# Kernel tuning notes

Measured on AMD Instinct MI355X. Metric: run time of the kernel, lower is better.

Reference implementation:

```python
import jax, jax.numpy as jnp
import numpy as np

B, S, D = 128, 1024, 256
K = 512  # num_clusters


def setup_inputs() -> dict:
    key = jax.random.key(0)
    k1, = jax.random.split(key, 1)
    inputs = jax.random.normal(k1, (B, S, D), dtype=jnp.float32)
    # init centroids as the first K data points so no cluster is empty
    centroids = inputs.reshape(-1, D)[:K]
    return {"inputs": inputs, "centroids": centroids}


def reference(inputs, centroids):
    d = inputs.shape[-1]
    k = centroids.shape[0]
    x = inputs.reshape(-1, d)                      # [N, D]
    # squared euclidean distances via GEMM decomposition (avoids N x K x D tensor)
    x2 = jnp.sum(x * x, axis=1, keepdims=True)     # [N, 1]
    c2 = jnp.sum(centroids * centroids, axis=1)    # [K]
    dist = x2 - 2.0 * (x @ centroids.T) + c2       # [N, K]
    idx = jnp.argmin(dist, axis=-1)                # [N]
    clusters = jax.nn.one_hot(idx, k, dtype=x.dtype)   # [N, K]
    counts = jnp.sum(clusters, axis=0)             # [K]
    sums = jnp.einsum('nk,nd->kd', clusters, x)    # [K, D] scatter-reduce as GEMM
    new_centroids = sums / counts[:, None]         # [K, D]
    updated_centroids = 0.9 * centroids + 0.1 * new_centroids  # EMA update
    clusters_out = clusters.reshape(inputs.shape[:-1] + (k,))  # [B, S, K]
    return clusters_out, updated_centroids
```

## Files before the change

### kernel.cpp

```cpp
#include <hip/hip_runtime.h>
#include <hip/hip_fp16.h>

#define NPTS 131072
#define DIM  256
#define KTOT 512
#define GAP_PAIR 0.2f
#define GAP_FULL 0.4f

typedef unsigned short u16;
typedef _Float16 half8 __attribute__((ext_vector_type(8)));
typedef float floatx4 __attribute__((ext_vector_type(4)));

union F16U { _Float16 f; unsigned short u; };

#define WS_MAIN_NEED 8394816u

__device__ __forceinline__ void ins2(float v, int k, float& B, int& KB, float& S, int& KS) {
  if (v < B || (v == B && k < KB)) { S = B; KS = KB; B = v; KB = k; }
  else if (v < S || (v == S && k < KS)) { S = v; KS = k; }
}

__global__ __launch_bounds__(64)
void c2_kernel(const float* __restrict__ c, double* __restrict__ c2) {
  int k = blockIdx.x;
  int lane = threadIdx.x;
  const float* row = c + (size_t)k * DIM;
  double s = 0.0;
#pragma unroll
  for (int r = 0; r < DIM / 64; ++r) {
    float v = row[r * 64 + lane];
    s += (double)v * (double)v;
  }
#pragma unroll
  for (int off = 32; off > 0; off >>= 1) s += __shfl_down(s, off);
  if (lane == 0) c2[k] = s;
}

__global__ __launch_bounds__(64)
void prep_c_kernel(const float* __restrict__ c, double* __restrict__ c2,
                   u16* __restrict__ Ch, float* __restrict__ cT) {
  int k = blockIdx.x, lane = threadIdx.x;
  const float* row = c + (size_t)k * DIM;
  float4 v = ((const float4*)row)[lane];
  double s = (double)v.x * v.x + (double)v.y * v.y + (double)v.z * v.z + (double)v.w * v.w;
#pragma unroll
  for (int off = 32; off > 0; off >>= 1) s += __shfl_down(s, off);
  if (lane == 0) c2[k] = s;
  cT[(size_t)(lane * 4 + 0) * KTOT + k] = v.x;
  cT[(size_t)(lane * 4 + 1) * KTOT + k] = v.y;
  cT[(size_t)(lane * 4 + 2) * KTOT + k] = v.z;
  cT[(size_t)(lane * 4 + 3) * KTOT + k] = v.w;
  int cg = lane >> 1, h = lane & 1;
  int kc = cg >> 3, cc = cg & 7;
  union { _Float16 hh[4]; ushort4 u; } cvt;
  cvt.hh[0] = (_Float16)v.x; cvt.hh[1] = (_Float16)v.y;
  cvt.hh[2] = (_Float16)v.z; cvt.hh[3] = (_Float16)v.w;
  *(ushort4*)(Ch + (size_t)k * DIM + kc * 64 + (size_t)(cc ^ (k & 7)) * 8 + h * 4) = cvt.u;
}

__device__ __forceinline__ void load_lds16(const void* g, void* l) {
  __builtin_amdgcn_global_load_lds((const __attribute__((address_space(1))) void*)g,
                                   (__attribute__((address_space(3))) void*)l, 16, 0, 0);
}

__global__ __launch_bounds__(256)
void gemm_topk_kernel(const float* __restrict__ x, const u16* __restrict__ Ch,
                      const double* __restrict__ c2,
                      float* __restrict__ pv1, int* __restrict__ pkk, unsigned* __restrict__ pgg) {
  __shared__ __align__(16) u16 Ah[128 * 64];
  __shared__ __align__(16) u16 Bh[128 * 64];
  __shared__ float mb[128][2], msv[128][2], mbf[128];
  __shared__ int mkb[128][2], mks[128][2], scnt[128][2];

  const int tid = threadIdx.x;
  const int bx = blockIdx.x;
  const int nblk = (bx >> 3) & 3;
  const int mblk = (bx & 7) + ((bx >> 5) << 3);
  const int m0 = mblk * 128, n0 = nblk * 128;
  const int w = tid >> 6, lane = tid & 63;
  const int wm = (w & 1) * 64, wn = (w >> 1) * 64;
  const int lm = lane & 15, quad = lane >> 4;

  floatx4 acc[4][4] = {};

  for (int kc = 0; kc < 4; ++kc) {
    const int k0 = kc * 64;
    __syncthreads();
#pragma unroll
    for (int i = 0; i < 4; ++i) {
      int s = i * 256 + tid;
      int row = s >> 3, pos = s & 7;
      size_t go = (size_t)(n0 + row) * DIM + k0 + pos * 8;
      load_lds16(Ch + go, Bh + (size_t)s * 8);
    }
#pragma unroll
    for (int i = 0; i < 4; ++i) {
      int s = i * 256 + tid;
      int row = s >> 3, kg = s & 7;
      const float4* gx = (const float4*)(x + (size_t)(m0 + row) * DIM + k0 + kg * 8);
      float4 f0 = gx[0], f1 = gx[1];
      float fv[8] = {f0.x, f0.y, f0.z, f0.w, f1.x, f1.y, f1.z, f1.w};
      half8 hv;
#pragma unroll
      for (int e = 0; e < 8; ++e) hv[e] = (_Float16)fv[e];
      int pos = kg ^ (row & 7);
      *(half8*)(Ah + (size_t)row * 64 + pos * 8) = hv;
    }
    __syncthreads();

#pragma unroll
    for (int s = 0; s < 2; ++s) {
      half8 ah[4], bh[4];
#pragma unroll
      for (int t = 0; t < 4; ++t) {
        int m = wm + t * 16 + lm;
        int pa = ((s * 4 + quad) ^ (m & 7)) * 8;
        ah[t] = *(const half8*)(Ah + (size_t)m * 64 + pa);
        int n = wn + t * 16 + lm;
        int pb = ((s * 4 + quad) ^ (n & 7)) * 8;
        bh[t] = *(const half8*)(Bh + (size_t)n * 64 + pb);
      }
#pragma unroll
      for (int mt = 0; mt < 4; ++mt)
#pragma unroll
        for (int nt = 0; nt < 4; ++nt)
          acc[mt][nt] = __builtin_amdgcn_mfma_f32_16x16x32_f16(ah[mt], bh[nt], acc[mt][nt], 0, 0, 0);
    }
  }

  float c2f[4];
#pragma unroll
  for (int nt = 0; nt < 4; ++nt) c2f[nt] = (float)c2[n0 + wn + nt * 16 + lm];

  __syncthreads();
#pragma unroll
  for (int mt = 0; mt < 4; ++mt)
#pragma unroll
    for (int r = 0; r < 4; ++r) {
      float bv = 1e30f, sv = 1e30f;
      int bk = 0x7fffffff, sk = 0x7fffffff;
#pragma unroll
      for (int nt = 0; nt < 4; ++nt) {
        float v = c2f[nt] - 2.0f * acc[mt][nt][r];
        int n = n0 + wn + nt * 16 + lm;
        if (v < bv || (v == bv && n < bk)) { sv = bv; sk = bk; bv = v; bk = n; }
        else if (v < sv || (v == sv && n < sk)) { sv = v; sk = n; }
      }
#pragma unroll
      for (int off = 1; off < 16; off <<= 1) {
        float ov = __shfl_xor(bv, off), osv = __shfl_xor(sv, off);
        int ok = __shfl_xor(bk, off), osk = __shfl_xor(sk, off);
        if (ov < bv || (ov == bv && ok < bk)) {
          if (bv < osv || (bv == osv && bk < osk)) { sv = bv; sk = bk; }
          else { sv = osv; sk = osk; }
          bv = ov; bk = ok;
        } else if (ov < sv || (ov == sv && ok < sk)) { sv = ov; sk = ok; }
      }
      if (lm == 0) {
        int mr = wm + mt * 16 + quad * 4 + r;
        int sl = w >> 1;
        mb[mr][sl] = bv; mkb[mr][sl] = bk; msv[mr][sl] = sv; mks[mr][sl] = sk;
      }
    }
  __syncthreads();
  if (tid < 128) {
    float B = mb[tid][0], S = msv[tid][0];
    int KB = mkb[tid][0], KS = mks[tid][0];
    ins2(mb[tid][1], mkb[tid][1], B, KB, S, KS);
    ins2(msv[tid][1], mks[tid][1], B, KB, S, KS);
    mb[tid][0] = B; mkb[tid][0] = KB; msv[tid][0] = S; mks[tid][0] = KS;
    mbf[tid] = B;
  }
  __syncthreads();
#pragma unroll
  for (int mt = 0; mt < 4; ++mt)
#pragma unroll
    for (int r = 0; r < 4; ++r) {
      int mr = wm + mt * 16 + quad * 4 + r;
      float thr = mbf[mr] + GAP_FULL;
      int cnt = 0;
#pragma unroll
      for (int nt = 0; nt < 4; ++nt)
        cnt += (c2f[nt] - 2.0f * acc[mt][nt][r] < thr) ? 1 : 0;
#pragma unroll
      for (int off = 1; off < 16; off <<= 1) cnt += __shfl_xor(cnt, off);
      if (lm == 0) scnt[mr][w >> 1] = cnt;
    }
  __syncthreads();
  if (tid < 128) {
    float B = mb[tid][0], S = msv[tid][0];
    int KB = mkb[tid][0], KS = mks[tid][0];
    int C = scnt[tid][0] + scnt[tid][1];
    int m = m0 + tid;
    F16U cv; cv.f = (_Float16)(S - B);
    pv1[(size_t)nblk * NPTS + m] = B;
    pkk[(size_t)nblk * NPTS + m] = KB | (KS << 16);
    pgg[(size_t)nblk * NPTS + m] = (unsigned)cv.u | ((unsigned)C << 16);
  }
}

__global__ __launch_bounds__(256)
void combine_kernel(const float* __restrict__ pv1, const int* __restrict__ pkk,
                    const unsigned* __restrict__ pgg, int* __restrict__ idx,
                    int* __restrict__ flagcnt, int* __restrict__ flaglist,
                    int* __restrict__ counts) {
  __shared__ int h[KTOT];
  int t = threadIdx.x;
#pragma unroll
  for (int i = 0; i < KTOT / 256; ++i) h[i * 256 + t] = 0;
  __syncthreads();
  int m = blockIdx.x * 256 + t;
  float B = 1e30f, S = 1e30f;
  int KB = 0x7fffffff, KS = 0x7fffffff;
  float bb[4]; int cc[4];
#pragma unroll
  for (int b = 0; b < 4; ++b) {
    float bv = pv1[(size_t)b * NPTS + m];
    int kk = pkk[(size_t)b * NPTS + m];
    unsigned gg = pgg[(size_t)b * NPTS + m];
    int kb_ = kk & 0xffff, ks_ = (kk >> 16) & 0xffff;
    F16U cv; cv.u = (unsigned short)(gg & 0xffffu);
    float sv = bv + (float)cv.f;
    bb[b] = bv; cc[b] = (int)(gg >> 16);
    ins2(bv, kb_, B, KB, S, KS);
    ins2(sv, ks_, B, KB, S, KS);
  }
  idx[m] = KB;
  atomicAdd(&h[KB], 1);
  int tot = 0;
#pragma unroll
  for (int b = 0; b < 4; ++b)
    if (bb[b] < B + GAP_FULL) tot += cc[b];
  if (tot >= 3) {
    int p = atomicAdd(&flagcnt[0], 1);
    if (p < 32768) flaglist[p] = m;
  } else if (tot == 2 && (S - B) < GAP_PAIR) {
    int p = atomicAdd(&flagcnt[1], 1);
    if (p < 32768) {
      flaglist[32768 + p] = m;
      flaglist[65536 + p] = KB | (KS << 16);
    }
  }
  __syncthreads();
#pragma unroll
  for (int i = 0; i < KTOT / 256; ++i) {
    int v = h[i * 256 + t];
    if (v) atomicAdd(&counts[i * 256 + t], v);
  }
}

__global__ __launch_bounds__(256)
void pair_refine_kernel(const float* __restrict__ x, const float* __restrict__ c,
                        const double* __restrict__ c2, const int* __restrict__ flagcnt,
                        const int* __restrict__ flaglist, int* __restrict__ idx,
                        int* __restrict__ counts) {
  int cnt = *(volatile const int*)(flagcnt + 1);
  const int w = threadIdx.x >> 6, lane = threadIdx.x & 63;
  for (int e = blockIdx.x * 4 + w; e < cnt; e += gridDim.x * 4) {
    int m = flaglist[32768 + e];
    int kk = flaglist[65536 + e];
    int ka = kk & 0xffff, kb = (kk >> 16) & 0xffff;
    float4 xv = ((const float4*)(x + (size_t)m * DIM))[lane];
    float4 av = ((const float4*)(c + (size_t)ka * DIM))[lane];
    float4 bv = ((const float4*)(c + (size_t)kb * DIM))[lane];
    float fa = fmaf(xv.x, av.x, fmaf(xv.y, av.y, fmaf(xv.z, av.z, xv.w * av.w)));
    float fb = fmaf(xv.x, bv.x, fmaf(xv.y, bv.y, fmaf(xv.z, bv.z, xv.w * bv.w)));
    double da = (double)fa, db = (double)fb;
#pragma unroll
    for (int off = 32; off > 0; off >>= 1) {
      da += __shfl_down(da, off);
      db += __shfl_down(db, off);
    }
    if (lane == 0) {
      double sa = c2[ka] - 2.0 * da, sb = c2[kb] - 2.0 * db;
      int wk = (sb < sa || (sb == sa && kb < ka)) ? kb : ka;
      if (wk != ka) {
        idx[m] = wk;
        atomicSub(&counts[ka], 1);
        atomicAdd(&counts[wk], 1);
      }
    }
  }
}

__global__ __launch_bounds__(256)
void full_refine_kernel(const float* __restrict__ x, const float* __restrict__ cT,
                        const double* __restrict__ c2, const int* __restrict__ flagcnt,
                        const int* __restrict__ flaglist, int* __restrict__ idx,
                        int* __restrict__ counts) {
  __shared__ __align__(16) float xs[DIM];
  __shared__ double rv[256];
  __shared__ int rk[256];
  int cnt = *(volatile const int*)flagcnt;
  const int ka = threadIdx.x, kb = threadIdx.x + 256;
  for (int i = blockIdx.x; i < cnt; i += gridDim.x) {
    __syncthreads();
    int m = flaglist[i];
    if (threadIdx.x < 64)
      ((float4*)xs)[threadIdx.x] = ((const float4*)(x + (size_t)m * DIM))[threadIdx.x];
    __syncthreads();
    double da = 0.0, db = 0.0;
#pragma unroll
    for (int dc = 0; dc < 8; ++dc) {
      float fa = 0.0f, fb = 0.0f;
#pragma unroll
      for (int d4 = 0; d4 < 8; ++d4) {
        float4 xv = ((const float4*)xs)[dc * 8 + d4];
        const float* ct0 = cT + (size_t)(dc * 32 + d4 * 4) * KTOT;
        fa = fmaf(xv.x, ct0[ka], fa);            fb = fmaf(xv.x, ct0[kb], fb);
        fa = fmaf(xv.y, ct0[KTOT + ka], fa);     fb = fmaf(xv.y, ct0[KTOT + kb], fb);
        fa = fmaf(xv.z, ct0[2 * KTOT + ka], fa); fb = fmaf(xv.z, ct0[2 * KTOT + kb], fb);
        fa = fmaf(xv.w, ct0[3 * KTOT + ka], fa); fb = fmaf(xv.w, ct0[3 * KTOT + kb], fb);
      }
      da += (double)fa; db += (double)fb;
    }
    double sa = c2[ka] - 2.0 * da, sb = c2[kb] - 2.0 * db;
    double bestv; int bestk;
    if (sa <= sb) { bestv = sa; bestk = ka; }
    else          { bestv = sb; bestk = kb; }
    rv[threadIdx.x] = bestv; rk[threadIdx.x] = bestk;
    __syncthreads();
    for (int off = 128; off > 0; off >>= 1) {
      if (threadIdx.x < off) {
        double v = rv[threadIdx.x + off]; int kk = rk[threadIdx.x + off];
        if (v < rv[threadIdx.x] || (v == rv[threadIdx.x] && kk < rk[threadIdx.x])) {
          rv[threadIdx.x] = v; rk[threadIdx.x] = kk;
        }
      }
      __syncthreads();
    }
    if (threadIdx.x == 0) {
      int bk = rk[0];
      int old = idx[m];
      if (bk != old) {
        idx[m] = bk;
        atomicSub(&counts[old], 1);
        atomicAdd(&counts[bk], 1);
      }
    }
  }
}

__global__ __launch_bounds__(256)
void onehot_kernel(const int* __restrict__ idx, float* __restrict__ out) {
  __shared__ int bk[32];
  int b = blockIdx.x;
  if (threadIdx.x < 32) bk[threadIdx.x] = idx[b * 32 + threadIdx.x];
  __syncthreads();
  float4* o = (float4*)(out + (size_t)b * 32 * KTOT);
#pragma unroll
  for (int j = 0; j < 16; ++j) {
    int f4 = j * 256 + threadIdx.x;
    int p = f4 >> 7;
    int n4 = (f4 & 127) * 4;
    int k = bk[p];
    float4 v;
    v.x = (k == n4 + 0) ? 1.0f : 0.0f;
    v.y = (k == n4 + 1) ? 1.0f : 0.0f;
    v.z = (k == n4 + 2) ? 1.0f : 0.0f;
    v.w = (k == n4 + 3) ? 1.0f : 0.0f;
    o[f4] = v;
  }
}

__global__ __launch_bounds__(512)
void scan_kernel(const int* __restrict__ counts, int* __restrict__ offsets,
                 int* __restrict__ cursors) {
  __shared__ int s[KTOT];
  int t = threadIdx.x;
  int mine = counts[t];
  s[t] = mine;
  __syncthreads();
  for (int off = 1; off < KTOT; off <<= 1) {
    int v = (t >= off) ? s[t - off] : 0;
    __syncthreads();
    s[t] += v;
    __syncthreads();
  }
  int excl = s[t] - mine;
  offsets[t] = excl;
  cursors[t] = excl;
  if (t == KTOT - 1) offsets[KTOT] = s[t];
}

__global__ __launch_bounds__(256)
void scatter_kernel(const int* __restrict__ idx, int* __restrict__ cursors,
                    int* __restrict__ plist) {
  int base = blockIdx.x * 1024 + threadIdx.x;
#pragma unroll
  for (int j = 0; j < 4; ++j) {
    int n = base + j * 256;
    int k = idx[n];
    int pos = atomicAdd(&cursors[k], 1);
    plist[pos] = n;
  }
}

__global__ __launch_bounds__(256)
void gathersum_flat_kernel(const float* __restrict__ x, const int* __restrict__ plist,
                           const int* __restrict__ offsets, float* __restrict__ sums) {
  __shared__ int offs[KTOT + 1];
  for (int t = threadIdx.x; t < KTOT + 1; t += 256) offs[t] = offsets[t];
  __syncthreads();
  const int w = threadIdx.x >> 6, lane = threadIdx.x & 63;
  const int wid = blockIdx.x * 4 + w;
  const int p0 = wid * 32, p1 = p0 + 32;

  int lo = 0, hi = KTOT;
  while (hi - lo > 1) { int mid = (lo + hi) >> 1; if (offs[mid] <= p0) lo = mid; else hi = mid; }
  int k = lo;

  float4 acc = make_float4(0.f, 0.f, 0.f, 0.f);
  bool any = false;
#pragma unroll 4
  for (int i = p0; i < p1; ++i) {
    while (i >= offs[k + 1]) {
      if (any) {
        float* dst = sums + (size_t)k * DIM + lane * 4;
        atomicAdd(dst + 0, acc.x); atomicAdd(dst + 1, acc.y);
        atomicAdd(dst + 2, acc.z); atomicAdd(dst + 3, acc.w);
        acc = make_float4(0.f, 0.f, 0.f, 0.f);
        any = false;
      }
      ++k;
    }
    int pid = plist[i];
    float4 v = ((const float4*)x)[(size_t)pid * 64 + lane];
    acc.x += v.x; acc.y += v.y; acc.z += v.z; acc.w += v.w;
    any = true;
  }
  if (any) {
    float* dst = sums + (size_t)k * DIM + lane * 4;
    atomicAdd(dst + 0, acc.x); atomicAdd(dst + 1, acc.y);
    atomicAdd(dst + 2, acc.z); atomicAdd(dst + 3, acc.w);
  }
}

__global__ __launch_bounds__(256)
void ema_kernel(const float* __restrict__ c, const float* __restrict__ sums,
                const int* __restrict__ counts, float* __restrict__ outc) {
  int k = blockIdx.x;
  int d = threadIdx.x;
  float cnt = (float)counts[k];
  size_t o = (size_t)k * DIM + d;
  float nc = sums[o] / cnt;
  outc[o] = 0.9f * c[o] + 0.1f * nc;
}

#define GB 4
#define SLICES 8
__global__ __launch_bounds__(256)
void sums_kernel(const float* __restrict__ x, const int* __restrict__ idx,
                 float* __restrict__ sums, int* __restrict__ counts) {
  const int groups = KTOT / GB;
  const int group = blockIdx.x % groups;
  const int slice = blockIdx.x / groups;
  const int kg0 = group * GB;
  const int tid = threadIdx.x;
  const int lane = tid & 63;
  const int w = tid >> 6;
  const int per_slice = NPTS / SLICES;
  const int nbeg = slice * per_slice;

  float4 acc[GB];
  int cnt[GB];
#pragma unroll
  for (int j = 0; j < GB; ++j) { acc[j] = make_float4(0.f, 0.f, 0.f, 0.f); cnt[j] = 0; }

  for (int it = 0; it < per_slice; it += 256) {
    int n = nbeg + it + tid;
    int k = idx[n];
#pragma unroll
    for (int j = 0; j < GB; ++j) {
      unsigned long long m = __ballot(k == kg0 + j);
      while (m) {
        int src = __ffsll((unsigned long long)m) - 1;
        int nn = __shfl(n, src);
        float4 v = ((const float4*)(x + (size_t)nn * DIM))[lane];
        acc[j].x += v.x; acc[j].y += v.y; acc[j].z += v.z; acc[j].w += v.w;
        cnt[j]++;
        m &= (m - 1);
      }
    }
  }

  __shared__ __align__(16) float lacc[4][GB][DIM];
  __shared__ int lcnt[4][GB];
#pragma unroll
  for (int j = 0; j < GB; ++j) ((float4*)&lacc[w][j][0])[lane] = acc[j];
  if (lane == 0) {
#pragma unroll
    for (int j = 0; j < GB; ++j) lcnt[w][j] = cnt[j];
  }
  __syncthreads();
#pragma unroll
  for (int j = 0; j < GB; ++j) {
    float s = lacc[0][j][tid] + lacc[1][j][tid] + lacc[2][j][tid] + lacc[3][j][tid];
    atomicAdd(&sums[(size_t)(kg0 + j) * DIM + tid], s);
  }
  if (tid < GB) {
    int ct = lcnt[0][tid] + lcnt[1][tid] + lcnt[2][tid] + lcnt[3][tid];
    atomicAdd(&counts[kg0 + tid], ct);
  }
}

#define MP 64
#define KT 64
#define DT 32
__global__ __launch_bounds__(256, 2)
void assign_kernel_r1(const float* __restrict__ x, const float* __restrict__ c,
                      const double* __restrict__ c2, float* __restrict__ out,
                      int* __restrict__ idx_out) {
  __shared__ __align__(16) float xs[DIM * MP];
  __shared__ __align__(16) float cs[DT * KT];
  const int tid = threadIdx.x;
  const int p0 = blockIdx.x * MP;
  const int tp = tid & 15;
  const int tk = tid >> 4;
  {
    const int p = tid >> 2;
    const int dg = tid & 3;
    const float4* x4 = (const float4*)(x + (size_t)(p0 + p) * DIM);
#pragma unroll
    for (int r = 0; r < 16; ++r) {
      int d4 = r * 4 + dg;
      float4 v = x4[d4];
      int dbase = d4 * 4;
      xs[(dbase + 0) * MP + p] = v.x;
      xs[(dbase + 1) * MP + p] = v.y;
      xs[(dbase + 2) * MP + p] = v.z;
      xs[(dbase + 3) * MP + p] = v.w;
    }
  }
  double best[4]; int bestk[4];
#pragma unroll
  for (int i = 0; i < 4; ++i) { best[i] = 1e300; bestk[i] = 0; }
  for (int kc = 0; kc < KTOT / KT; ++kc) {
    const int k0 = kc * KT;
    double dacc[4][4];
#pragma unroll
    for (int i = 0; i < 4; ++i)
#pragma unroll
      for (int j = 0; j < 4; ++j) dacc[i][j] = 0.0;
    for (int dc = 0; dc < DIM / DT; ++dc) {
      __syncthreads();
      {
        const int kl = tid >> 2;
        const int dg = tid & 3;
        const float4* c4 = (const float4*)(c + (size_t)(k0 + kl) * DIM + dc * DT);
#pragma unroll
        for (int h = 0; h < 2; ++h) {
          int dq = h * 4 + dg;
          float4 v = c4[dq];
          int dbase = dq * 4;
          cs[(dbase + 0) * KT + kl] = v.x;
          cs[(dbase + 1) * KT + kl] = v.y;
          cs[(dbase + 2) * KT + kl] = v.z;
          cs[(dbase + 3) * KT + kl] = v.w;
        }
      }
      __syncthreads();
      float acc[4][4];
#pragma unroll
      for (int i = 0; i < 4; ++i)
#pragma unroll
        for (int j = 0; j < 4; ++j) acc[i][j] = 0.0f;
#pragma unroll
      for (int d = 0; d < DT; ++d) {
        float4 xv = ((const float4*)(xs + (size_t)(dc * DT + d) * MP))[tp];
        float4 cv = ((const float4*)(cs + (size_t)d * KT))[tk];
        float xa[4] = {xv.x, xv.y, xv.z, xv.w};
        float ca[4] = {cv.x, cv.y, cv.z, cv.w};
#pragma unroll
        for (int i = 0; i < 4; ++i)
#pragma unroll
          for (int j = 0; j < 4; ++j) acc[i][j] = fmaf(xa[i], ca[j], acc[i][j]);
      }
#pragma unroll
      for (int i = 0; i < 4; ++i)
#pragma unroll
        for (int j = 0; j < 4; ++j) dacc[i][j] += (double)acc[i][j];
    }
#pragma unroll
    for (int j = 0; j < 4; ++j) {
      int k = k0 + tk * 4 + j;
      double c2v = c2[k];
#pragma unroll
      for (int i = 0; i < 4; ++i) {
        double s = c2v - 2.0 * dacc[i][j];
        if (s < best[i]) { best[i] = s; bestk[i] = k; }
      }
    }
  }
  __syncthreads();
  double* redv = (double*)cs;
  int* redk = (int*)xs;
  int* bk = (int*)xs + 1024;
#pragma unroll
  for (int i = 0; i < 4; ++i) {
    int p = tp * 4 + i;
    redv[tk * MP + p] = best[i];
    redk[tk * MP + p] = bestk[i];
  }
  __syncthreads();
  if (tid < MP) {
    int p = tid;
    double bv = redv[p]; int bkk = redk[p];
#pragma unroll
    for (int t = 1; t < 16; ++t) {
      double v = redv[t * MP + p]; int kk = redk[t * MP + p];
      if (v < bv || (v == bv && kk < bkk)) { bv = v; bkk = kk; }
    }
    bk[p] = bkk;
    idx_out[p0 + p] = bkk;
  }
  __syncthreads();
  float* orow = out + (size_t)p0 * KTOT;
  for (int l = tid; l < MP * KTOT; l += 256) {
    int p = l >> 9;
    int k = l & (KTOT - 1);
    orow[l] = (k == bk[p]) ? 1.0f : 0.0f;
  }
}

extern "C" void kernel_launch(void* const* d_in, const int* in_sizes, int n_in,
                              void* d_out, int out_size, void* d_ws, size_t ws_size,
                              hipStream_t stream) {
  const float* x = (const float*)d_in[0];
  const float* c = (const float*)d_in[1];
  float* out = (float*)d_out;
  float* outc = out + (size_t)NPTS * KTOT;

  char* ws = (char*)d_ws;

  if (ws_size >= WS_MAIN_NEED) {
    double* c2   = (double*)(ws + 0);
    u16* Ch      = (u16*)(ws + 4096);
    int* idx     = (int*)(ws + 528384);
    float* pv1   = (float*)(ws + 1052672);
    int* pkk     = (int*)(ws + 3149824);
    unsigned* pgg= (unsigned*)(ws + 5246976);
    float* sums  = (float*)(ws + 7344128);
    int* counts  = (int*)(ws + 7868416);
    int* flagcnt = (int*)(ws + 7870464);
    int* flaglist= (int*)(ws + 7870528);
    int* offsets = (int*)(ws + 1052672);
    int* cursors = (int*)(ws + 1052672 + 4096);
    int* plist   = (int*)(ws + 5246976);
    float* cT    = (float*)((char*)out + 134217728);

    hipMemsetAsync(sums, 0, (size_t)(KTOT * DIM + KTOT) * 4, stream);
    hipMemsetAsync(flagcnt, 0, 64, stream);
    prep_c_kernel<<<KTOT, 64, 0, stream>>>(c, c2, Ch, cT);
    gemm_topk_kernel<<<4096, 256, 0, stream>>>(x, Ch, c2, pv1, pkk, pgg);
    combine_kernel<<<NPTS / 256, 256, 0, stream>>>(pv1, pkk, pgg, idx, flagcnt, flaglist, counts);
    full_refine_kernel<<<256, 256, 0, stream>>>(x, cT, c2, flagcnt, flaglist, idx, counts);
    pair_refine_kernel<<<256, 256, 0, stream>>>(x, c, c2, flagcnt, flaglist, idx, counts);
    onehot_kernel<<<NPTS / 32, 256, 0, stream>>>(idx, out);
    scan_kernel<<<1, 512, 0, stream>>>(counts, offsets, cursors);
    scatter_kernel<<<NPTS / 1024, 256, 0, stream>>>(idx, cursors, plist);
    gathersum_flat_kernel<<<NPTS / 32 / 4, 256, 0, stream>>>(x, plist, offsets, sums);
    ema_kernel<<<KTOT, DIM, 0, stream>>>(c, sums, counts, outc);
  } else {
    double* c2  = (double*)ws;
    int* idx    = (int*)(ws + 4096);
    float* sums = (float*)(ws + 4096 + 524288);
    int* counts = (int*)(ws + 4096 + 524288 + 524288);
    hipMemsetAsync(sums, 0, (size_t)(KTOT * DIM + KTOT) * 4, stream);
    c2_kernel<<<KTOT, 64, 0, stream>>>(c, c2);
    assign_kernel_r1<<<NPTS / MP, 256, 0, stream>>>(x, c, c2, out, idx);
    sums_kernel<<<(KTOT / GB) * SLICES, 256, 0, stream>>>(x, idx, sums, counts);
    ema_kernel<<<KTOT, DIM, 0, stream>>>(c, sums, counts, outc);
  }
}
```

Baseline: 830.0 us.

## Stage GEMM scores in LDS for top-3 row scan and fold flag reset into prep

The GEMM epilogue now writes the distance tile into shared memory, reusing the A/B staging buffers, in two halves. Threads scan contiguous row segments to find the top-3 candidates instead of running shuffle-based top-2 reductions plus a second thresholded counting pass. The partial output now carries the third-best gap in place of a near-threshold count, and combine rebuilds the count from the three values. The flagcnt memset is folded into prep_c_kernel to save one launch. The changes add extra barriers and LDS traffic, and the near-ambiguity count changes from an exact count to an approximation capped at three per block.

```diff
diff --git a/kernel.cpp b/kernel.cpp
--- a/kernel.cpp
+++ b/kernel.cpp
@@ -38,8 +38,9 @@
 
 __global__ __launch_bounds__(64)
 void prep_c_kernel(const float* __restrict__ c, double* __restrict__ c2,
-                   u16* __restrict__ Ch, float* __restrict__ cT) {
+                   u16* __restrict__ Ch, float* __restrict__ cT, int* __restrict__ flagcnt) {
   int k = blockIdx.x, lane = threadIdx.x;
+  if (k == 0 && lane < 16) flagcnt[lane] = 0;
   const float* row = c + (size_t)k * DIM;
   float4 v = ((const float4*)row)[lane];
   double s = (double)v.x * v.x + (double)v.y * v.y + (double)v.z * v.z + (double)v.w * v.w;
@@ -67,10 +68,12 @@
 void gemm_topk_kernel(const float* __restrict__ x, const u16* __restrict__ Ch,
                       const double* __restrict__ c2,
                       float* __restrict__ pv1, int* __restrict__ pkk, unsigned* __restrict__ pgg) {
-  __shared__ __align__(16) u16 Ah[128 * 64];
-  __shared__ __align__(16) u16 Bh[128 * 64];
-  __shared__ float mb[128][2], msv[128][2], mbf[128];
-  __shared__ int mkb[128][2], mks[128][2], scnt[128][2];
+  __shared__ __align__(16) unsigned char smem[33792];
+  __shared__ float rB[128], rS[128], rT[128];
+  __shared__ int rKB[128], rKS[128];
+  u16* Ah = (u16*)smem;
+  u16* Bh = Ah + 8192;
+  float* sc = (float*)smem;
 
   const int tid = threadIdx.x;
   const int bx = blockIdx.x;
@@ -132,70 +135,77 @@
 #pragma unroll
   for (int nt = 0; nt < 4; ++nt) c2f[nt] = (float)c2[n0 + wn + nt * 16 + lm];
 
-  __syncthreads();
-#pragma unroll
-  for (int mt = 0; mt < 4; ++mt)
-#pragma unroll
-    for (int r = 0; r < 4; ++r) {
-      float bv = 1e30f, sv = 1e30f;
-      int bk = 0x7fffffff, sk = 0x7fffffff;
-#pragma unroll
-      for (int nt = 0; nt < 4; ++nt) {
-        float v = c2f[nt] - 2.0f * acc[mt][nt][r];
-        int n = n0 + wn + nt * 16 + lm;
-        if (v < bv || (v == bv && n < bk)) { sv = bv; sk = bk; bv = v; bk = n; }
-        else if (v < sv || (v == sv && n < sk)) { sv = v; sk = n; }
-      }
-#pragma unroll
-      for (int off = 1; off < 16; off <<= 1) {
-        float ov = __shfl_xor(bv, off), osv = __shfl_xor(sv, off);
-        int ok = __shfl_xor(bk, off), osk = __shfl_xor(sk, off);
-        if (ov < bv || (ov == bv && ok < bk)) {
-          if (bv < osv || (bv == osv && bk < osk)) { sv = bv; sk = bk; }
-          else { sv = osv; sk = osk; }
-          bv = ov; bk = ok;
-        } else if (ov < sv || (ov == sv && ok < sk)) { sv = ov; sk = ok; }
-      }
-      if (lm == 0) {
-        int mr = wm + mt * 16 + quad * 4 + r;
-        int sl = w >> 1;
-        mb[mr][sl] = bv; mkb[mr][sl] = bk; msv[mr][sl] = sv; mks[mr][sl] = sk;
-      }
-    }
+  for (int half = 0; half < 2; ++half) {
+    __syncthreads();
+#pragma unroll
+    for (int mt2 = 0; mt2 < 2; ++mt2) {
+      int mt = half * 2 + mt2;
+      int hrow0 = (wm >> 1) + mt2 * 16 + quad * 4;
+#pragma unroll
+      for (int r = 0; r < 4; ++r)
+#pragma unroll
+        for (int nt = 0; nt < 4; ++nt)
+          sc[(hrow0 + r) * 132 + wn + nt * 16 + lm] = c2f[nt] - 2.0f * acc[mt][nt][r];
+    }
+    __syncthreads();
+    {
+      int hrow = tid >> 2, seg = tid & 3;
+      float B = 1e30f, S = 1e30f, T = 1e30f;
+      int KB = -1, KS = -1;
+      const float4* rp = (const float4*)(sc + hrow * 132 + seg * 32);
+#pragma unroll
+      for (int j = 0; j < 8; ++j) {
+        float4 v4 = rp[j];
+        float va[4] = {v4.x, v4.y, v4.z, v4.w};
+#pragma unroll
+        for (int e = 0; e < 4; ++e) {
+          float v = va[e];
+          int n = seg * 32 + j * 4 + e;
+          if (v < B) { T = S; S = B; KS = KB; B = v; KB = n; }
+          else if (v < S) { T = S; S = v; KS = n; }
+          else if (v < T) T = v;
+        }
+      }
+      __syncthreads();
+      float* sb = sc;
+      int base = (hrow * 4 + seg) * 5;
+      sb[base + 0] = B;
+      sb[base + 1] = __int_as_float(KB);
+      sb[base + 2] = S;
+      sb[base + 3] = __int_as_float(KS);
+      sb[base + 4] = T;
+    }
+    __syncthreads();
+    if (tid < 64) {
+      float* sb = sc;
+      float B = 1e30f, S = 1e30f, T = 1e30f;
+      int KB = -1, KS = -1;
+#pragma unroll
+      for (int s2 = 0; s2 < 4; ++s2) {
+        const float* e = sb + (tid * 4 + s2) * 5;
+        float b2 = e[0]; int kb2 = __float_as_int(e[1]);
+        float s3 = e[2]; int ks2 = __float_as_int(e[3]);
+        float t2 = e[4];
+        if (b2 < B) { T = S; S = B; KS = KB; B = b2; KB = kb2; }
+        else if (b2 < S) { T = S; S = b2; KS = kb2; }
+        else if (b2 < T) T = b2;
+        if (s3 < S) { T = S; S = s3; KS = ks2; }
+        else if (s3 < T) T = s3;
+        if (t2 < T) T = t2;
+      }
+      int m = (tid < 32 ? tid : tid + 32) + half * 32;
+      rB[m] = B; rKB[m] = KB; rS[m] = S; rKS[m] = KS; rT[m] = T;
+    }
+  }
   __syncthreads();
   if (tid < 128) {
-    float B = mb[tid][0], S = msv[tid][0];
-    int KB = mkb[tid][0], KS = mks[tid][0];
-    ins2(mb[tid][1], mkb[tid][1], B, KB, S, KS);
-    ins2(msv[tid][1], mks[tid][1], B, KB, S, KS);
-    mb[tid][0] = B; mkb[tid][0] = KB; msv[tid][0] = S; mks[tid][0] = KS;
-    mbf[tid] = B;
-  }
-  __syncthreads();
-#pragma unroll
-  for (int mt = 0; mt < 4; ++mt)
-#pragma unroll
-    for (int r = 0; r < 4; ++r) {
-      int mr = wm + mt * 16 + quad * 4 + r;
-      float thr = mbf[mr] + GAP_FULL;
-      int cnt = 0;
-#pragma unroll
-      for (int nt = 0; nt < 4; ++nt)
-        cnt += (c2f[nt] - 2.0f * acc[mt][nt][r] < thr) ? 1 : 0;
-#pragma unroll
-      for (int off = 1; off < 16; off <<= 1) cnt += __shfl_xor(cnt, off);
-      if (lm == 0) scnt[mr][w >> 1] = cnt;
-    }
-  __syncthreads();
-  if (tid < 128) {
-    float B = mb[tid][0], S = msv[tid][0];
-    int KB = mkb[tid][0], KS = mks[tid][0];
-    int C = scnt[tid][0] + scnt[tid][1];
+    float B = rB[tid], S = rS[tid], T = rT[tid];
     int m = m0 + tid;
-    F16U cv; cv.f = (_Float16)(S - B);
+    F16U g1; g1.f = (_Float16)(S - B);
+    F16U g2; g2.f = (_Float16)(T - B);
     pv1[(size_t)nblk * NPTS + m] = B;
-    pkk[(size_t)nblk * NPTS + m] = KB | (KS << 16);
-    pgg[(size_t)nblk * NPTS + m] = (unsigned)cv.u | ((unsigned)C << 16);
+    pkk[(size_t)nblk * NPTS + m] = (rKB[tid] + n0) | ((rKS[tid] + n0) << 16);
+    pgg[(size_t)nblk * NPTS + m] = (unsigned)g1.u | ((unsigned)g2.u << 16);
   }
 }
 
@@ -212,25 +222,27 @@
   int m = blockIdx.x * 256 + t;
   float B = 1e30f, S = 1e30f;
   int KB = 0x7fffffff, KS = 0x7fffffff;
-  float bb[4]; int cc[4];
+  float bb[4], ss[4], tt[4];
 #pragma unroll
   for (int b = 0; b < 4; ++b) {
     float bv = pv1[(size_t)b * NPTS + m];
     int kk = pkk[(size_t)b * NPTS + m];
     unsigned gg = pgg[(size_t)b * NPTS + m];
     int kb_ = kk & 0xffff, ks_ = (kk >> 16) & 0xffff;
-    F16U cv; cv.u = (unsigned short)(gg & 0xffffu);
-    float sv = bv + (float)cv.f;
-    bb[b] = bv; cc[b] = (int)(gg >> 16);
+    F16U u1; u1.u = (unsigned short)(gg & 0xffffu);
+    F16U u2; u2.u = (unsigned short)(gg >> 16);
+    float sv = bv + (float)u1.f, tv = bv + (float)u2.f;
+    bb[b] = bv; ss[b] = sv; tt[b] = tv;
     ins2(bv, kb_, B, KB, S, KS);
     ins2(sv, ks_, B, KB, S, KS);
   }
   idx[m] = KB;
   atomicAdd(&h[KB], 1);
+  float thr = B + GAP_FULL;
   int tot = 0;
 #pragma unroll
   for (int b = 0; b < 4; ++b)
-    if (bb[b] < B + GAP_FULL) tot += cc[b];
+    tot += ((bb[b] < thr) ? 1 : 0) + ((ss[b] < thr) ? 1 : 0) + ((tt[b] < thr) ? 1 : 0);
   if (tot >= 3) {
     int p = atomicAdd(&flagcnt[0], 1);
     if (p < 32768) flaglist[p] = m;
@@ -650,8 +662,7 @@
     float* cT    = (float*)((char*)out + 134217728);
 
     hipMemsetAsync(sums, 0, (size_t)(KTOT * DIM + KTOT) * 4, stream);
-    hipMemsetAsync(flagcnt, 0, 64, stream);
-    prep_c_kernel<<<KTOT, 64, 0, stream>>>(c, c2, Ch, cT);
+    prep_c_kernel<<<KTOT, 64, 0, stream>>>(c, c2, Ch, cT, flagcnt);
     gemm_topk_kernel<<<4096, 256, 0, stream>>>(x, Ch, c2, pv1, pkk, pgg);
     combine_kernel<<<NPTS / 256, 256, 0, stream>>>(pv1, pkk, pgg, idx, flagcnt, flaglist, counts);
     full_refine_kernel<<<256, 256, 0, stream>>>(x, cT, c2, flagcnt, flaglist, idx, counts);
```

New measurement: 703.9 us. 15.2% less time.
